# Kernel tuning notes

Measured on AMD Instinct MI355X. Metric: run time of the kernel, lower is better.

Reference implementation:

```python
import jax, jax.numpy as jnp
import numpy as np

B, S, D, H = 1, 2048, 1024, 16
HD = D // H
S_SLOPE = 10.0      # soft_thres_layer s
C_MASK = -10000.0   # soft_thres_layer c == masked_bias
ALPHA = 0.0         # config.threshold
W_STD = 0.02        # GPT2 init std for weights


def setup_inputs() -> dict:
    key = jax.random.key(0)
    k1, k2, k3 = jax.random.split(key, 3)
    return {
        "hidden_states": jax.random.normal(k1, (B, S, D), dtype=jnp.float32),
        "c_attn_w": jax.random.normal(k2, (D, 3 * D), dtype=jnp.float32) * W_STD,
        "c_attn_b": jnp.zeros((3 * D,), dtype=jnp.float32),
        "c_proj_w": jax.random.normal(k3, (D, D), dtype=jnp.float32) * W_STD,
        "c_proj_b": jnp.zeros((D,), dtype=jnp.float32),
    }


def reference(hidden_states, c_attn_w, c_attn_b, c_proj_w, c_proj_b):
    # Conv1D: x @ w + b (GPT2 convention: weight is [in, out])
    qkv = hidden_states @ c_attn_w + c_attn_b            # [B,S,3D]
    q, k, v = jnp.split(qkv, 3, axis=-1)

    def split_heads(x):
        return x.reshape(B, S, H, HD).transpose(0, 2, 1, 3)  # [B,H,S,hd]

    q, k, v = split_heads(q), split_heads(k), split_heads(v)

    # prun path: NO 1/sqrt(d) scaling (skipped when self.prun is True)
    w = jnp.einsum("bhqd,bhkd->bhqk", q, k)              # [B,H,S,S]

    causal = jnp.tril(jnp.ones((S, S), dtype=bool))[None, None]
    w = jnp.where(causal, w, C_MASK)

    # soft-threshold pruning: smoothly pushes scores below alpha toward c=-10000
    w = C_MASK + (w - C_MASK) * jax.nn.sigmoid(S_SLOPE * (w - ALPHA))

    a = jax.nn.softmax(w, axis=-1)                        # attn_dropout = identity (eval)
    out = jnp.einsum("bhqk,bhkd->bhqd", a, v)             # [B,H,S,hd]
    out = out.transpose(0, 2, 1, 3).reshape(B, S, D)      # merge heads
    return out @ c_proj_w + c_proj_b                      # resid_dropout = identity
```

## Files before the change

kernel.cpp:

```cpp
#include <hip/hip_runtime.h>


#define S_LEN 2048
#define DM    1024
#define NH    16
#define HD    64
#define NQKV  3072
#define SLOPE 10.0f
#define CMASK -10000.0f
#define QROWS 32

typedef short s16x4 __attribute__((ext_vector_type(4)));
typedef short s16x8 __attribute__((ext_vector_type(8)));
typedef float f32x4 __attribute__((ext_vector_type(4)));

#define MFMA16(a,b,c) __builtin_amdgcn_mfma_f32_16x16x32_bf16(a,b,c,0,0,0)
#define GLDS16(g,l) __builtin_amdgcn_global_load_lds( \
    (const __attribute__((address_space(1))) void*)(g), \
    (__attribute__((address_space(3))) void*)(l), 16, 0, 0)

__device__ __forceinline__ short f2bf(float f){
    unsigned u = __float_as_uint(f);
    u += 0x7fffu + ((u >> 16) & 1u);
    return (short)(u >> 16);
}
struct bfpair { short hi, lo; };
__device__ __forceinline__ bfpair split_bf(float x){
    bfpair r; r.hi = f2bf(x);
    float fh = __uint_as_float(((unsigned)(unsigned short)r.hi) << 16);
    r.lo = f2bf(x - fh);
    return r;
}

template<int ROWS, int THREADS>
__device__ __forceinline__ void stage_tile(const short* gbase, int rstride,
                                           short* lds, int tid){
#pragma unroll
    for (int it = 0; it < ROWS*8/THREADS; ++it){
        int s = it*THREADS + tid;
        int row = s >> 3, grp = s & 7;
        const short* src = gbase + (size_t)row*rstride + ((grp ^ (row & 7)) << 3);
        GLDS16(src, lds + (size_t)s*8);
    }
}
__device__ __forceinline__ s16x8 frag(const short* lds, int row, int kg){
    return *(const s16x8*)&lds[row*64 + ((kg ^ (row & 7)) << 3)];
}

template<bool WSPLIT, bool QKV>
__global__ __launch_bounds__(256)
void gemm_kern(const short* __restrict__ Ahg, const short* __restrict__ Alg,
               const short* __restrict__ Bhg, const short* __restrict__ Blg,
               const float* __restrict__ bias,
               short* __restrict__ o0h, short* __restrict__ o0l,
               short* __restrict__ o1h, short* __restrict__ o1l,
               short* __restrict__ o2,  float* __restrict__ oproj)
{
    __shared__ __align__(16) short Ah_s[128*64];
    __shared__ __align__(16) short Al_s[128*64];
    __shared__ __align__(16) short Bh_s[128*64];
    __shared__ __align__(16) short Bl_s[WSPLIT ? 128*64 : 8];

    const int tid = threadIdx.x, lane = tid & 63, wid = tid >> 6;
    const int lr = lane & 15, lg = lane >> 4;
    const int brow = blockIdx.y*128, bcol = blockIdx.x*128;
    const int wm = (wid >> 1)*64, wn = (wid & 1)*64;

    f32x4 acc[4][4];
#pragma unroll
    for (int m = 0; m < 4; ++m)
#pragma unroll
        for (int n = 0; n < 4; ++n) acc[m][n] = (f32x4){0.f,0.f,0.f,0.f};

    for (int k0 = 0; k0 < DM; k0 += 64){
        stage_tile<128,256>(Ahg + (size_t)brow*DM + k0, DM, Ah_s, tid);
        stage_tile<128,256>(Alg + (size_t)brow*DM + k0, DM, Al_s, tid);
        stage_tile<128,256>(Bhg + (size_t)bcol*DM + k0, DM, Bh_s, tid);
        if constexpr (WSPLIT)
            stage_tile<128,256>(Blg + (size_t)bcol*DM + k0, DM, Bl_s, tid);
        __syncthreads();
#pragma unroll
        for (int kc = 0; kc < 2; ++kc){
            s16x8 ah[4], al[4], bh[4], bl[4];
#pragma unroll
            for (int m = 0; m < 4; ++m){
                ah[m] = frag(Ah_s, wm + m*16 + lr, kc*4 + lg);
                al[m] = frag(Al_s, wm + m*16 + lr, kc*4 + lg);
            }
#pragma unroll
            for (int n = 0; n < 4; ++n){
                bh[n] = frag(Bh_s, wn + n*16 + lr, kc*4 + lg);
                if constexpr (WSPLIT)
                    bl[n] = frag(Bl_s, wn + n*16 + lr, kc*4 + lg);
            }
#pragma unroll
            for (int m = 0; m < 4; ++m)
#pragma unroll
                for (int n = 0; n < 4; ++n){
                    acc[m][n] = MFMA16(ah[m], bh[n], acc[m][n]);
                    if constexpr (WSPLIT)
                        acc[m][n] = MFMA16(ah[m], bl[n], acc[m][n]);
                    acc[m][n] = MFMA16(al[m], bh[n], acc[m][n]);
                }
        }
        __syncthreads();
    }

    const int sec = bcol >> 10;
#pragma unroll
    for (int m = 0; m < 4; ++m)
#pragma unroll
        for (int n = 0; n < 4; ++n){
            int row  = brow + wm + m*16 + lg*4;
            int gcol = bcol + wn + n*16 + lr;
            float bv = bias[gcol];
#pragma unroll
            for (int v = 0; v < 4; ++v){
                float val = acc[m][n][v] + bv;
                if constexpr (QKV){
                    int col1 = gcol & 1023;
                    size_t o = (size_t)(row + v)*DM + col1;
                    if (sec == 0){ bfpair p = split_bf(val); o0h[o] = p.hi; o0l[o] = p.lo; }
                    else if (sec == 1){ bfpair p = split_bf(val); o1h[o] = p.hi; o1l[o] = p.lo; }
                    else { o2[o] = f2bf(val); }
                } else {
                    oproj[(size_t)(row + v)*DM + gcol] = val;
                }
            }
        }
}

__global__ __launch_bounds__(256)
void split_f32(const float* __restrict__ x, short* __restrict__ h,
               short* __restrict__ l, int n4)
{
    int i = blockIdx.x*256 + threadIdx.x;
    if (i >= n4) return;
    float4 v = *(const float4*)&x[(size_t)i*4];
    bfpair a = split_bf(v.x), b = split_bf(v.y), c = split_bf(v.z), d = split_bf(v.w);
    s16x4 hv, lv;
    hv.x = a.hi; hv.y = b.hi; hv.z = c.hi; hv.w = d.hi;
    lv.x = a.lo; lv.y = b.lo; lv.z = c.lo; lv.w = d.lo;
    *(s16x4*)&h[(size_t)i*4] = hv;
    *(s16x4*)&l[(size_t)i*4] = lv;
}

template<bool SPL>
__global__ __launch_bounds__(256)
void wtrans(const float* __restrict__ W, int N, short* __restrict__ Th,
            short* __restrict__ Tl)
{
    __shared__ float t[64][65];
    const int tid = threadIdx.x;
    const int tn = blockIdx.x*64, tk = blockIdx.y*64;
#pragma unroll
    for (int it = 0; it < 4; ++it){
        int idx = tid + it*256;
        int r = idx >> 4, c4 = (idx & 15)*4;
        float4 v = *(const float4*)&W[(size_t)(tk + r)*N + tn + c4];
        t[r][c4] = v.x; t[r][c4+1] = v.y; t[r][c4+2] = v.z; t[r][c4+3] = v.w;
    }
    __syncthreads();
#pragma unroll
    for (int it = 0; it < 4; ++it){
        int idx = tid + it*256;
        int n = idx >> 4, c4 = (idx & 15)*4;
        s16x4 hv, lv;
#pragma unroll
        for (int j = 0; j < 4; ++j){
            bfpair p = split_bf(t[c4+j][n]);
            hv[j] = p.hi; lv[j] = p.lo;
        }
        *(s16x4*)&Th[(size_t)(tn + n)*DM + tk + c4] = hv;
        if constexpr (SPL) *(s16x4*)&Tl[(size_t)(tn + n)*DM + tk + c4] = lv;
    }
}

__global__ __launch_bounds__(256)
void vtrans(const short* __restrict__ Vb, short* __restrict__ Vt)
{
    __shared__ short t[64][66];
    const int tid = threadIdx.x;
    const int td = blockIdx.x*64, ts = blockIdx.y*64;
#pragma unroll
    for (int it = 0; it < 4; ++it){
        int idx = tid + it*256;
        int r = idx >> 4, c4 = (idx & 15)*4;
        s16x4 v = *(const s16x4*)&Vb[(size_t)(ts + r)*DM + td + c4];
        t[r][c4] = v.x; t[r][c4+1] = v.y; t[r][c4+2] = v.z; t[r][c4+3] = v.w;
    }
    __syncthreads();
#pragma unroll
    for (int it = 0; it < 4; ++it){
        int idx = tid + it*256;
        int n = idx >> 4, c4 = (idx & 15)*4;
        s16x4 o;
#pragma unroll
        for (int j = 0; j < 4; ++j) o[j] = t[c4+j][n];
        *(s16x4*)&Vt[(size_t)(td + n)*S_LEN + ts + c4] = o;
    }
}

__global__ __launch_bounds__(128)
void attn_fwd(const short* __restrict__ Qh, const short* __restrict__ Ql,
              const short* __restrict__ Kh, const short* __restrict__ Kl,
              const short* __restrict__ Vt,
              short* __restrict__ Oh, short* __restrict__ Ol)
{
    __shared__ __align__(16) short qh_s[QROWS*64], ql_s[QROWS*64];
    __shared__ __align__(16) short kh_s[64*64], kl_s[64*64];
    __shared__ __align__(16) short vt_s[64*64];
    __shared__ __align__(16) short Ps[2][16*72];

    const int bx = blockIdx.x, h = blockIdx.y;
    const int lid = bx + (h << 6);
    const int qt = ((lid >> 8) & 1) ? bx : (S_LEN/QROWS - 1) - bx;
    const int diag = (qt*QROWS + QROWS - 1) >> 6;

    const int tid = threadIdx.x, lane = tid & 63, wid = tid >> 6;
    const int lr = lane & 15, lg = lane >> 4;

    stage_tile<QROWS,128>(Qh + (size_t)(qt*QROWS)*DM + h*HD, DM, qh_s, tid);
    stage_tile<QROWS,128>(Ql + (size_t)(qt*QROWS)*DM + h*HD, DM, ql_s, tid);
    __syncthreads();

    s16x8 aqh[2], aql[2];
#pragma unroll
    for (int kc = 0; kc < 2; ++kc){
        aqh[kc] = frag(qh_s, wid*16 + lr, kc*4 + lg);
        aql[kc] = frag(ql_s, wid*16 + lr, kc*4 + lg);
    }

    float m_run[4], l_run[4];
    f32x4 acc_o[4];
#pragma unroll
    for (int v = 0; v < 4; ++v){ m_run[v] = -1e30f; l_run[v] = 0.f; }
#pragma unroll
    for (int n = 0; n < 4; ++n) acc_o[n] = (f32x4){0.f,0.f,0.f,0.f};

    const int qrow = qt*QROWS + wid*16 + lg*4;

    for (int kvb = 0; kvb < S_LEN/64; ++kvb){
        stage_tile<64,128>(Kh + (size_t)(kvb*64)*DM + h*HD, DM, kh_s, tid);
        stage_tile<64,128>(Kl + (size_t)(kvb*64)*DM + h*HD, DM, kl_s, tid);
        stage_tile<64,128>(Vt + (size_t)(h*HD)*S_LEN + kvb*64, S_LEN, vt_s, tid);
        __syncthreads();

        f32x4 sc[4];
#pragma unroll
        for (int n = 0; n < 4; ++n) sc[n] = (f32x4){0.f,0.f,0.f,0.f};
#pragma unroll
        for (int kc = 0; kc < 2; ++kc)
#pragma unroll
            for (int n = 0; n < 4; ++n){
                s16x8 bkh = frag(kh_s, n*16 + lr, kc*4 + lg);
                s16x8 bkl = frag(kl_s, n*16 + lr, kc*4 + lg);
                sc[n] = MFMA16(aqh[kc], bkh, sc[n]);
                sc[n] = MFMA16(aqh[kc], bkl, sc[n]);
                sc[n] = MFMA16(aql[kc], bkh, sc[n]);
            }

        float p[4][4], tmax[4];
#pragma unroll
        for (int v = 0; v < 4; ++v) tmax[v] = -1e30f;
        if (kvb >= diag){
#pragma unroll
            for (int n = 0; n < 4; ++n){
                int key = kvb*64 + n*16 + lr;
#pragma unroll
                for (int v = 0; v < 4; ++v){
                    float w;
                    if (key > qrow + v) w = CMASK;
                    else {
                        float sv = sc[n][v];
                        float sig = 1.f / (1.f + __expf(-SLOPE*sv));
                        w = CMASK + (sv - CMASK)*sig;
                    }
                    p[n][v] = w;
                    tmax[v] = fmaxf(tmax[v], w);
                }
            }
        } else {
#pragma unroll
            for (int n = 0; n < 4; ++n)
#pragma unroll
                for (int v = 0; v < 4; ++v){
                    float sv = sc[n][v];
                    float sig = 1.f / (1.f + __expf(-SLOPE*sv));
                    float w = CMASK + (sv - CMASK)*sig;
                    p[n][v] = w;
                    tmax[v] = fmaxf(tmax[v], w);
                }
        }
#pragma unroll
        for (int v = 0; v < 4; ++v)
#pragma unroll
            for (int msk = 1; msk < 16; msk <<= 1)
                tmax[v] = fmaxf(tmax[v], __shfl_xor(tmax[v], msk, 64));

        float scale[4], rsum[4];
#pragma unroll
        for (int v = 0; v < 4; ++v){
            float mn = fmaxf(m_run[v], tmax[v]);
            scale[v] = __expf(m_run[v] - mn);
            m_run[v] = mn;
            rsum[v] = 0.f;
        }
#pragma unroll
        for (int n = 0; n < 4; ++n)
#pragma unroll
            for (int v = 0; v < 4; ++v){
                float e = __expf(p[n][v] - m_run[v]);
                p[n][v] = e;
                rsum[v] += e;
            }
#pragma unroll
        for (int v = 0; v < 4; ++v){
#pragma unroll
            for (int msk = 1; msk < 16; msk <<= 1)
                rsum[v] += __shfl_xor(rsum[v], msk, 64);
            l_run[v] = l_run[v]*scale[v] + rsum[v];
        }
#pragma unroll
        for (int n = 0; n < 4; ++n)
#pragma unroll
            for (int v = 0; v < 4; ++v) acc_o[n][v] *= scale[v];

#pragma unroll
        for (int n = 0; n < 4; ++n)
#pragma unroll
            for (int v = 0; v < 4; ++v)
                Ps[wid][(lg*4 + v)*72 + 16*n + lr] = f2bf(p[n][v]);
        asm volatile("s_waitcnt lgkmcnt(0)" ::: "memory");

        s16x8 pa0 = *(const s16x8*)&Ps[wid][lr*72 + lg*8];
        s16x8 pa1 = *(const s16x8*)&Ps[wid][lr*72 + 32 + lg*8];
#pragma unroll
        for (int n = 0; n < 4; ++n){
            s16x8 bv0 = frag(vt_s, 16*n + lr, lg);
            s16x8 bv1 = frag(vt_s, 16*n + lr, 4 + lg);
            acc_o[n] = MFMA16(pa0, bv0, acc_o[n]);
            acc_o[n] = MFMA16(pa1, bv1, acc_o[n]);
        }

        int ok = (kvb >= diag);
#pragma unroll
        for (int v = 0; v < 4; ++v)
            ok = ok && (m_run[v] > CMASK + 100.f);
        if (__syncthreads_and(ok)) break;
    }

#pragma unroll
    for (int n = 0; n < 4; ++n)
#pragma unroll
        for (int v = 0; v < 4; ++v){
            int row = qrow + v;
            int col = h*HD + 16*n + lr;
            bfpair p = split_bf(acc_o[n][v] / l_run[v]);
            Oh[(size_t)row*DM + col] = p.hi;
            Ol[(size_t)row*DM + col] = p.lo;
        }
}

extern "C" void kernel_launch(void* const* d_in, const int* in_sizes, int n_in,
                              void* d_out, int out_size, void* d_ws, size_t ws_size,
                              hipStream_t stream)
{
    (void)in_sizes; (void)n_in; (void)out_size; (void)ws_size;
    const float* hs   = (const float*)d_in[0];
    const float* wqkv = (const float*)d_in[1];
    const float* bqkv = (const float*)d_in[2];
    const float* wprj = (const float*)d_in[3];
    const float* bprj = (const float*)d_in[4];

    char* p = (char*)d_ws;
    short* Ahg  = (short*)(p + (0ull  << 20));
    short* Alg  = (short*)(p + (4ull  << 20));
    short* WqTh = (short*)(p + (8ull  << 20));
    short* WqTl = (short*)(p + (14ull << 20));
    short* Qhg  = (short*)(p + (20ull << 20));
    short* Qlg  = (short*)(p + (24ull << 20));
    short* Khg  = (short*)(p + (28ull << 20));
    short* Klg  = (short*)(p + (32ull << 20));
    short* Vbg  = (short*)(p + (36ull << 20));
    short* Vtg  = (short*)(p + (40ull << 20));
    short* Oh = Ahg, * Ol = Alg;
    short* WpT = WqTh;

    split_f32<<<S_LEN*DM/4/256, 256, 0, stream>>>(hs, Ahg, Alg, S_LEN*DM/4);
    wtrans<true><<<dim3(NQKV/64, DM/64), 256, 0, stream>>>(wqkv, NQKV, WqTh, WqTl);

    gemm_kern<true, true><<<dim3(NQKV/128, S_LEN/128), 256, 0, stream>>>(
        Ahg, Alg, WqTh, WqTl, bqkv, Qhg, Qlg, Khg, Klg, Vbg, nullptr);

    wtrans<false><<<dim3(DM/64, DM/64), 256, 0, stream>>>(wprj, DM, WpT, nullptr);
    vtrans<<<dim3(DM/64, S_LEN/64), 256, 0, stream>>>(Vbg, Vtg);

    attn_fwd<<<dim3(S_LEN/QROWS, NH), 128, 0, stream>>>(Qhg, Qlg, Khg, Klg, Vtg, Oh, Ol);

    gemm_kern<false, false><<<dim3(DM/128, S_LEN/128), 256, 0, stream>>>(
        Oh, Ol, WpT, nullptr, bprj, nullptr, nullptr, nullptr, nullptr, nullptr,
        (float*)d_out);
}
```

Baseline: 195.2 us.

## Replace masked-tail attention with suffix V sums and register-fed single-wave blocks

```diff
diff --git a/kernel.cpp b/kernel.cpp
--- a/kernel.cpp
+++ b/kernel.cpp
@@ -8,7 +8,6 @@
 #define NQKV  3072
 #define SLOPE 10.0f
 #define CMASK -10000.0f
-#define QROWS 32
 
 typedef short s16x4 __attribute__((ext_vector_type(4)));
 typedef short s16x8 __attribute__((ext_vector_type(8)));
@@ -24,11 +23,13 @@
     u += 0x7fffu + ((u >> 16) & 1u);
     return (short)(u >> 16);
 }
+__device__ __forceinline__ float bf2f(short x){
+    return __uint_as_float(((unsigned)(unsigned short)x) << 16);
+}
 struct bfpair { short hi, lo; };
 __device__ __forceinline__ bfpair split_bf(float x){
     bfpair r; r.hi = f2bf(x);
-    float fh = __uint_as_float(((unsigned)(unsigned short)r.hi) << 16);
-    r.lo = f2bf(x - fh);
+    r.lo = f2bf(x - bf2f(r.hi));
     return r;
 }
 
@@ -53,7 +54,7 @@
                const short* __restrict__ Bhg, const short* __restrict__ Blg,
                const float* __restrict__ bias,
                short* __restrict__ o0h, short* __restrict__ o0l,
-               short* __restrict__ o1h, short* __restrict__ o1l,
+               short* __restrict__ o1h,
                short* __restrict__ o2,  float* __restrict__ oproj)
 {
     __shared__ __align__(16) short Ah_s[128*64];
@@ -121,7 +122,7 @@
                     int col1 = gcol & 1023;
                     size_t o = (size_t)(row + v)*DM + col1;
                     if (sec == 0){ bfpair p = split_bf(val); o0h[o] = p.hi; o0l[o] = p.lo; }
-                    else if (sec == 1){ bfpair p = split_bf(val); o1h[o] = p.hi; o1l[o] = p.lo; }
+                    else if (sec == 1){ o1h[o] = f2bf(val); }
                     else { o2[o] = f2bf(val); }
                 } else {
                     oproj[(size_t)(row + v)*DM + gcol] = val;
@@ -201,34 +202,51 @@
     }
 }
 
-__global__ __launch_bounds__(128)
+__global__ __launch_bounds__(64)
+void sv_partial(const short* __restrict__ Vb, float* __restrict__ PB)
+{
+    int b = blockIdx.x, h = blockIdx.y, d = threadIdx.x;
+    float s = 0.f;
+#pragma unroll 8
+    for (int k = 0; k < 64; ++k)
+        s += bf2f(Vb[(size_t)(b*64 + k)*DM + h*HD + d]);
+    PB[((size_t)h*32 + b)*64 + d] = s;
+}
+__global__ __launch_bounds__(64)
+void sv_suffix(const float* __restrict__ PB, float* __restrict__ SSV)
+{
+    int h = blockIdx.x, d = threadIdx.x;
+    float s = 0.f;
+    SSV[((size_t)h*33 + 32)*64 + d] = 0.f;
+    for (int b = 31; b >= 0; --b){
+        s += PB[((size_t)h*32 + b)*64 + d];
+        SSV[((size_t)h*33 + b)*64 + d] = s;
+    }
+}
+
+__global__ __launch_bounds__(64)
 void attn_fwd(const short* __restrict__ Qh, const short* __restrict__ Ql,
-              const short* __restrict__ Kh, const short* __restrict__ Kl,
-              const short* __restrict__ Vt,
+              const short* __restrict__ Kh, const short* __restrict__ Vt,
+              const float* __restrict__ SSV,
               short* __restrict__ Oh, short* __restrict__ Ol)
 {
-    __shared__ __align__(16) short qh_s[QROWS*64], ql_s[QROWS*64];
-    __shared__ __align__(16) short kh_s[64*64], kl_s[64*64];
-    __shared__ __align__(16) short vt_s[64*64];
-    __shared__ __align__(16) short Ps[2][16*72];
-
-    const int bx = blockIdx.x, h = blockIdx.y;
-    const int lid = bx + (h << 6);
-    const int qt = ((lid >> 8) & 1) ? bx : (S_LEN/QROWS - 1) - bx;
-    const int diag = (qt*QROWS + QROWS - 1) >> 6;
-
-    const int tid = threadIdx.x, lane = tid & 63, wid = tid >> 6;
-    const int lr = lane & 15, lg = lane >> 4;
-
-    stage_tile<QROWS,128>(Qh + (size_t)(qt*QROWS)*DM + h*HD, DM, qh_s, tid);
-    stage_tile<QROWS,128>(Ql + (size_t)(qt*QROWS)*DM + h*HD, DM, ql_s, tid);
-    __syncthreads();
-
+    __shared__ __align__(16) short Ps[16*72];
+
+    const int id = blockIdx.x;
+    const int h  = (id & 7) + 8*((id >> 3) & 1);
+    const int qt = 127 - (id >> 4);
+    const int diag = qt >> 2;
+
+    const int lane = threadIdx.x, lr = lane & 15, lg = lane >> 4;
+    const int qrow = qt*16 + lg*4;
+
+    const short* qbh = Qh + (size_t)(qt*16)*DM + h*HD;
+    const short* qbl = Ql + (size_t)(qt*16)*DM + h*HD;
     s16x8 aqh[2], aql[2];
 #pragma unroll
     for (int kc = 0; kc < 2; ++kc){
-        aqh[kc] = frag(qh_s, wid*16 + lr, kc*4 + lg);
-        aql[kc] = frag(ql_s, wid*16 + lr, kc*4 + lg);
+        aqh[kc] = *(const s16x8*)&qbh[(size_t)lr*DM + kc*32 + lg*8];
+        aql[kc] = *(const s16x8*)&qbl[(size_t)lr*DM + kc*32 + lg*8];
     }
 
     float m_run[4], l_run[4];
@@ -238,13 +256,17 @@
 #pragma unroll
     for (int n = 0; n < 4; ++n) acc_o[n] = (f32x4){0.f,0.f,0.f,0.f};
 
-    const int qrow = qt*QROWS + wid*16 + lg*4;
-
-    for (int kvb = 0; kvb < S_LEN/64; ++kvb){
-        stage_tile<64,128>(Kh + (size_t)(kvb*64)*DM + h*HD, DM, kh_s, tid);
-        stage_tile<64,128>(Kl + (size_t)(kvb*64)*DM + h*HD, DM, kl_s, tid);
-        stage_tile<64,128>(Vt + (size_t)(h*HD)*S_LEN + kvb*64, S_LEN, vt_s, tid);
-        __syncthreads();
+    const short* kb0 = Kh + (size_t)h*HD;
+    const short* vb0 = Vt + (size_t)(h*HD)*S_LEN;
+
+    for (int kvb = 0; kvb <= diag; ++kvb){
+        const short* kb = kb0 + (size_t)(kvb*64)*DM;
+        s16x8 bk[2][4];
+#pragma unroll
+        for (int kc = 0; kc < 2; ++kc)
+#pragma unroll
+            for (int n = 0; n < 4; ++n)
+                bk[kc][n] = *(const s16x8*)&kb[(size_t)(n*16 + lr)*DM + kc*32 + lg*8];
 
         f32x4 sc[4];
 #pragma unroll
@@ -253,17 +275,22 @@
         for (int kc = 0; kc < 2; ++kc)
 #pragma unroll
             for (int n = 0; n < 4; ++n){
-                s16x8 bkh = frag(kh_s, n*16 + lr, kc*4 + lg);
-                s16x8 bkl = frag(kl_s, n*16 + lr, kc*4 + lg);
-                sc[n] = MFMA16(aqh[kc], bkh, sc[n]);
-                sc[n] = MFMA16(aqh[kc], bkl, sc[n]);
-                sc[n] = MFMA16(aql[kc], bkh, sc[n]);
-            }
+                sc[n] = MFMA16(aqh[kc], bk[kc][n], sc[n]);
+                sc[n] = MFMA16(aql[kc], bk[kc][n], sc[n]);
+            }
+
+        const short* vb = vb0 + kvb*64;
+        s16x8 bv0[4], bv1[4];
+#pragma unroll
+        for (int n = 0; n < 4; ++n){
+            bv0[n] = *(const s16x8*)&vb[(size_t)(16*n + lr)*S_LEN + lg*8];
+            bv1[n] = *(const s16x8*)&vb[(size_t)(16*n + lr)*S_LEN + 32 + lg*8];
+        }
 
         float p[4][4], tmax[4];
 #pragma unroll
         for (int v = 0; v < 4; ++v) tmax[v] = -1e30f;
-        if (kvb >= diag){
+        if (kvb == diag){
 #pragma unroll
             for (int n = 0; n < 4; ++n){
                 int key = kvb*64 + n*16 + lr;
@@ -330,31 +357,40 @@
         for (int n = 0; n < 4; ++n)
 #pragma unroll
             for (int v = 0; v < 4; ++v)
-                Ps[wid][(lg*4 + v)*72 + 16*n + lr] = f2bf(p[n][v]);
+                Ps[(lg*4 + v)*72 + 16*n + lr] = f2bf(p[n][v]);
         asm volatile("s_waitcnt lgkmcnt(0)" ::: "memory");
 
-        s16x8 pa0 = *(const s16x8*)&Ps[wid][lr*72 + lg*8];
-        s16x8 pa1 = *(const s16x8*)&Ps[wid][lr*72 + 32 + lg*8];
+        s16x8 pa0 = *(const s16x8*)&Ps[lr*72 + lg*8];
+        s16x8 pa1 = *(const s16x8*)&Ps[lr*72 + 32 + lg*8];
 #pragma unroll
         for (int n = 0; n < 4; ++n){
-            s16x8 bv0 = frag(vt_s, 16*n + lr, lg);
-            s16x8 bv1 = frag(vt_s, 16*n + lr, 4 + lg);
-            acc_o[n] = MFMA16(pa0, bv0, acc_o[n]);
-            acc_o[n] = MFMA16(pa1, bv1, acc_o[n]);
-        }
-
-        int ok = (kvb >= diag);
-#pragma unroll
-        for (int v = 0; v < 4; ++v)
-            ok = ok && (m_run[v] > CMASK + 100.f);
-        if (__syncthreads_and(ok)) break;
+            acc_o[n] = MFMA16(pa0, bv0[n], acc_o[n]);
+            acc_o[n] = MFMA16(pa1, bv1[n], acc_o[n]);
+        }
+    }
+
+    {
+        const float* sv = SSV + ((size_t)h*33 + (diag + 1))*64;
+        float F = (float)(S_LEN - 64*(diag + 1));
+        float e[4];
+#pragma unroll
+        for (int v = 0; v < 4; ++v){
+            e[v] = __expf(CMASK - m_run[v]);
+            l_run[v] += e[v]*F;
+        }
+#pragma unroll
+        for (int n = 0; n < 4; ++n){
+            float svv = sv[16*n + lr];
+#pragma unroll
+            for (int v = 0; v < 4; ++v) acc_o[n][v] += e[v]*svv;
+        }
     }
 
 #pragma unroll
     for (int n = 0; n < 4; ++n)
 #pragma unroll
         for (int v = 0; v < 4; ++v){
-            int row = qrow + v;
+            int row = qt*16 + lg*4 + v;
             int col = h*HD + 16*n + lr;
             bfpair p = split_bf(acc_o[n][v] / l_run[v]);
             Oh[(size_t)row*DM + col] = p.hi;
@@ -381,9 +417,10 @@
     short* Qhg  = (short*)(p + (20ull << 20));
     short* Qlg  = (short*)(p + (24ull << 20));
     short* Khg  = (short*)(p + (28ull << 20));
-    short* Klg  = (short*)(p + (32ull << 20));
-    short* Vbg  = (short*)(p + (36ull << 20));
-    short* Vtg  = (short*)(p + (40ull << 20));
+    short* Vbg  = (short*)(p + (32ull << 20));
+    short* Vtg  = (short*)(p + (36ull << 20));
+    float* PB   = (float*)(p + (40ull << 20));
+    float* SSV  = (float*)(p + (41ull << 20));
     short* Oh = Ahg, * Ol = Alg;
     short* WpT = WqTh;
 
@@ -391,14 +428,16 @@
     wtrans<true><<<dim3(NQKV/64, DM/64), 256, 0, stream>>>(wqkv, NQKV, WqTh, WqTl);
 
     gemm_kern<true, true><<<dim3(NQKV/128, S_LEN/128), 256, 0, stream>>>(
-        Ahg, Alg, WqTh, WqTl, bqkv, Qhg, Qlg, Khg, Klg, Vbg, nullptr);
+        Ahg, Alg, WqTh, WqTl, bqkv, Qhg, Qlg, Khg, Vbg, nullptr);
 
     wtrans<false><<<dim3(DM/64, DM/64), 256, 0, stream>>>(wprj, DM, WpT, nullptr);
     vtrans<<<dim3(DM/64, S_LEN/64), 256, 0, stream>>>(Vbg, Vtg);
-
-    attn_fwd<<<dim3(S_LEN/QROWS, NH), 128, 0, stream>>>(Qhg, Qlg, Khg, Klg, Vtg, Oh, Ol);
+    sv_partial<<<dim3(32, NH), 64, 0, stream>>>(Vbg, PB);
+    sv_suffix<<<NH, 64, 0, stream>>>(PB, SSV);
+
+    attn_fwd<<<2048, 64, 0, stream>>>(Qhg, Qlg, Khg, Vtg, SSV, Oh, Ol);
 
     gemm_kern<false, false><<<dim3(DM/128, S_LEN/128), 256, 0, stream>>>(
-        Oh, Ol, WpT, nullptr, bprj, nullptr, nullptr, nullptr, nullptr, nullptr,
+        Oh, Ol, WpT, nullptr, bprj, nullptr, nullptr, nullptr, nullptr,
         (float*)d_out);
 }
```

Measured after the change: 173.3 us. 11.2% less time.
